# Performance work log

Measured on AMD Instinct MI355X. Metric: run time of the kernel, lower is better.

## Reference

```python
import jax, jax.numpy as jnp
import numpy as np

N_NODES = 50000
N_EDGES = 800000
HIDDEN = 128
NUM_RBF = 32
N_GRAPHS = 500
VOCAB = 100


def setup_inputs() -> dict:
    key = jax.random.key(0)
    ks = jax.random.split(key, 16)
    x = jax.random.randint(ks[0], (N_NODES,), 0, VOCAB)
    edge_index = jax.random.randint(ks[1], (2, N_EDGES), 0, N_NODES)
    edge_attr = jax.random.normal(ks[2], (N_EDGES, NUM_RBF), dtype=jnp.float32)
    batch = jnp.sort(jax.random.randint(ks[3], (N_NODES,), 0, N_GRAPHS))
    zdim = 2 * HIDDEN + NUM_RBF
    s = 1.0 / np.sqrt(zdim)
    params = {"emb": jax.random.normal(ks[4], (VOCAB, HIDDEN), dtype=jnp.float32)}
    for l, k0 in zip((1, 2, 3), (5, 8, 11)):
        params[f"Wf{l}"] = jax.random.uniform(ks[k0], (zdim, HIDDEN), minval=-s, maxval=s, dtype=jnp.float32)
        params[f"bf{l}"] = jnp.zeros((HIDDEN,), dtype=jnp.float32)
        params[f"Ws{l}"] = jax.random.uniform(ks[k0 + 1], (zdim, HIDDEN), minval=-s, maxval=s, dtype=jnp.float32)
        params[f"bs{l}"] = jnp.zeros((HIDDEN,), dtype=jnp.float32)
    sl = 1.0 / np.sqrt(HIDDEN)
    params["Wlin"] = jax.random.uniform(ks[14], (HIDDEN, HIDDEN), minval=-sl, maxval=sl, dtype=jnp.float32)
    params["blin"] = jnp.zeros((HIDDEN,), dtype=jnp.float32)
    return {"x": x, "edge_index": edge_index, "edge_attr": edge_attr, "batch": batch, **params}


def _cgconv(h, src, dst, edge_attr, Wf, bf, Ws, bs):
    # z = [x_i || x_j || e_ij]; i = target (dst), j = source (src)
    z = jnp.concatenate([h[dst], h[src], edge_attr], axis=-1)  # [E, 2H+D]
    msg = jax.nn.sigmoid(z @ Wf + bf) * jax.nn.softplus(z @ Ws + bs)  # [E, H]
    agg = jax.ops.segment_sum(msg, dst, num_segments=N_NODES)
    return h + agg


def reference(x, edge_index, edge_attr, batch, emb,
              Wf1, bf1, Ws1, bs1, Wf2, bf2, Ws2, bs2, Wf3, bf3, Ws3, bs3,
              Wlin, blin):
    src, dst = edge_index[0], edge_index[1]
    h = emb[x]  # [N, H]
    h = jax.nn.relu(_cgconv(h, src, dst, edge_attr, Wf1, bf1, Ws1, bs1))
    h = jax.nn.relu(_cgconv(h, src, dst, edge_attr, Wf2, bf2, Ws2, bs2))
    h = jax.nn.relu(_cgconv(h, src, dst, edge_attr, Wf3, bf3, Ws3, bs3))
    sums = jax.ops.segment_sum(h, batch, num_segments=N_GRAPHS)  # [G, H]
    counts = jax.ops.segment_sum(jnp.ones((N_NODES,), h.dtype), batch, num_segments=N_GRAPHS)
    pooled = sums / jnp.maximum(counts, 1.0)[:, None]
    return pooled @ Wlin + blin
```

## Files before the change

kernel.cpp:

```cpp
#include <hip/hip_runtime.h>
#include <hip/hip_bf16.h>
#include <hip/hip_fp16.h>
#include <cstdint>
#include <cstddef>

#define NNODES 50000
#define NEDGES 800000
#define HID 128
#define NRBF 32
#define NGRAPH 500
#define NB_SCAN 196
#define EPB 32
#define NEBLK (NEDGES / EPB)
#define SROW 130

typedef __attribute__((ext_vector_type(8))) short short8;
typedef __attribute__((ext_vector_type(4))) float f32x4;

__device__ inline short f2bf(float x) {
  __hip_bfloat16 b = __float2bfloat16(x);
  return *reinterpret_cast<short*>(&b);
}

__device__ inline unsigned int pk_bf16(float a, float b) {
  unsigned int r;
  asm("v_cvt_pk_bf16_f32 %0, %1, %2" : "=v"(r) : "v"(a), "v"(b));
  return r;
}
__device__ inline unsigned int pk_f16(float a, float b) {
  unsigned int r;
  asm("v_cvt_pkrtz_f16_f32 %0, %1, %2" : "=v"(r) : "v"(a), "v"(b));
  return r;
}
__device__ inline float aexp2(float x) {
  float r;
  asm("v_exp_f32 %0, %1" : "=v"(r) : "v"(x));
  return r;
}
__device__ inline float alog2(float x) {
  float r;
  asm("v_log_f32 %0, %1" : "=v"(r) : "v"(x));
  return r;
}

#define SC_F (-1.4426950408889634f)
#define SC_S (1.4426950408889634f)

__global__ void prep_all(
    const float* __restrict__ Wf0, const float* __restrict__ Ws0,
    const float* __restrict__ bf0, const float* __restrict__ bs0,
    const float* __restrict__ Wf1, const float* __restrict__ Ws1,
    const float* __restrict__ bf1, const float* __restrict__ bs1,
    const float* __restrict__ Wf2, const float* __restrict__ Ws2,
    const float* __restrict__ bf2, const float* __restrict__ bs2,
    unsigned short* __restrict__ WtB3, unsigned short* __restrict__ WnB3,
    float* __restrict__ biasv3) {
  const int l = blockIdx.y;
  const float* Wf = (l == 0) ? Wf0 : ((l == 1) ? Wf1 : Wf2);
  const float* Ws = (l == 0) ? Ws0 : ((l == 1) ? Ws1 : Ws2);
  const float* bf = (l == 0) ? bf0 : ((l == 1) ? bf1 : bf2);
  const float* bs = (l == 0) ? bs0 : ((l == 1) ? bs1 : bs2);
  unsigned short* WtB = WtB3 + l * 8192;
  unsigned short* WnB = WnB3 + l * 65536;
  float* biasv = biasv3 + l * 256;

  int i0 = blockIdx.x * blockDim.x + threadIdx.x;
  if (i0 < 8192) {
    int i = i0;
    int j = i & 7, lane = (i >> 3) & 63, t = i >> 9;
    int q = lane >> 4, n = lane & 15;
    int k = q * 8 + j, c = (t & 7) * 16 + n;
    const float* W = (t < 8) ? Wf : Ws;
    const float sc = (t < 8) ? SC_F : SC_S;
    WtB[i] = (unsigned short)f2bf(W[(size_t)(256 + k) * HID + c] * sc);
  } else if (i0 < 8192 + 65536) {
    int i = i0 - 8192;
    int j = i & 7;
    int lane = (i >> 3) & 63;
    int tk = (i >> 9) & 3;
    int tc = i >> 11;
    int q = lane >> 4, n = lane & 15;
    int k = tk * 32 + q * 8 + j;
    float v;
    int which;
    if (tc < 16) {
      int cc = tc * 16 + n;
      int c = cc >> 1;
      which = cc & 1;
      const float* W = which ? Ws : Wf;
      v = W[(size_t)k * HID + c];
    } else {
      int g = (tc - 16) >> 1;
      which = (tc - 16) & 1;
      int c = g * 16 + n;
      const float* W = which ? Ws : Wf;
      v = W[(size_t)(128 + k) * HID + c];
    }
    WnB[i] = (unsigned short)f2bf(v * (which ? SC_S : SC_F));
    if (i < 256) {
      int c2 = i >> 1, w2 = i & 1;
      biasv[i] = w2 ? bs[c2] * SC_S : bf[c2] * SC_F;
    }
  }
}

__global__ void deg_hist(const int* __restrict__ dst, int* __restrict__ deg) {
  int e = blockIdx.x * blockDim.x + threadIdx.x;
  if (e < NEDGES) atomicAdd(&deg[dst[e]], 1);
}

__global__ __launch_bounds__(256) void scan_block(const int* __restrict__ deg, int* __restrict__ bsum) {
  __shared__ int s[256];
  int i = blockIdx.x * 256 + threadIdx.x;
  s[threadIdx.x] = (i < NNODES) ? deg[i] : 0;
  __syncthreads();
  for (int off = 128; off > 0; off >>= 1) {
    if (threadIdx.x < off) s[threadIdx.x] += s[threadIdx.x + off];
    __syncthreads();
  }
  if (threadIdx.x == 0) bsum[blockIdx.x] = s[0];
}

__global__ __launch_bounds__(256) void scan_top(const int* __restrict__ bsum,
                                                int* __restrict__ bpre) {
  __shared__ int s[256];
  int t = threadIdx.x;
  int v = (t < NB_SCAN) ? bsum[t] : 0;
  s[t] = v;
  __syncthreads();
  for (int off = 1; off < 256; off <<= 1) {
    int u = (t >= off) ? s[t - off] : 0;
    __syncthreads();
    s[t] += u;
    __syncthreads();
  }
  if (t < NB_SCAN) bpre[t] = s[t] - v;
}

__global__ __launch_bounds__(256) void scan_final(const int* __restrict__ deg,
                                                  const int* __restrict__ bpre,
                                                  int* __restrict__ cursor) {
  __shared__ int s[256];
  int i = blockIdx.x * 256 + threadIdx.x;
  int v = (i < NNODES) ? deg[i] : 0;
  s[threadIdx.x] = v;
  __syncthreads();
  for (int off = 1; off < 256; off <<= 1) {
    int t = (threadIdx.x >= off) ? s[threadIdx.x - off] : 0;
    __syncthreads();
    s[threadIdx.x] += t;
    __syncthreads();
  }
  if (i < NNODES) cursor[i] = bpre[blockIdx.x] + s[threadIdx.x] - v;
}

__global__ void scatter_edges_pack(const int* __restrict__ src, const int* __restrict__ dst,
                                   const float* __restrict__ eattr, int* __restrict__ cursor,
                                   int2* __restrict__ se2, unsigned short* __restrict__ eaB) {
  int e = blockIdx.x * blockDim.x + threadIdx.x;
  if (e >= NEDGES) return;
  int d = dst[e];
  int pos = atomicAdd(&cursor[d], 1);
  se2[pos] = make_int2(src[e], d);
  const float* ep = eattr + (size_t)e * NRBF;
  unsigned short* op = eaB + (size_t)pos * NRBF;
#pragma unroll
  for (int part = 0; part < 4; ++part) {
    const float4 v0 = *(const float4*)&ep[part * 8];
    const float4 v1 = *(const float4*)&ep[part * 8 + 4];
    uint4 o;
    o.x = pk_bf16(v0.x, v0.y);
    o.y = pk_bf16(v0.z, v0.w);
    o.z = pk_bf16(v1.x, v1.y);
    o.w = pk_bf16(v1.z, v1.w);
    *(uint4*)&op[part * 8] = o;
  }
}

__global__ __launch_bounds__(256) void node_mfma(
    const int* __restrict__ x, const float* __restrict__ emb,
    float* __restrict__ h, float* __restrict__ agg,
    const unsigned short* __restrict__ WnB, const float* __restrict__ biasv,
    float* __restrict__ Pdst, unsigned int* __restrict__ Psrc, int mode, int N) {
  const int tid = threadIdx.x;
  const int wv = tid >> 6;
  const int lane = tid & 63;
  const int q = lane >> 4;
  const int n = lane & 15;
  const int nb = blockIdx.x * 32 + (wv >> 1) * 16;
  const int srcwave = wv & 1;
  const int ctile0 = srcwave * 16;

  const bool valid = (nb + n) < N;
  int anode = nb + n;
  if (anode >= N) anode = N - 1;
  float* hp = h + (size_t)anode * HID;

  short8 a[4];
  if (mode == 0) {
    const float* ep = emb + (size_t)x[anode] * HID;
#pragma unroll
    for (int kt = 0; kt < 4; ++kt) {
      const float4 e0 = *(const float4*)&ep[kt * 32 + q * 8];
      const float4 e1 = *(const float4*)&ep[kt * 32 + q * 8 + 4];
      if (valid && !srcwave) {
        *(float4*)&hp[kt * 32 + q * 8] = e0;
        *(float4*)&hp[kt * 32 + q * 8 + 4] = e1;
      }
      union { short8 s8; unsigned int u32[4]; } au;
      au.u32[0] = pk_bf16(e0.x, e0.y);
      au.u32[1] = pk_bf16(e0.z, e0.w);
      au.u32[2] = pk_bf16(e1.x, e1.y);
      au.u32[3] = pk_bf16(e1.z, e1.w);
      a[kt] = au.s8;
    }
  } else {
    float* ap = agg + (size_t)anode * HID;
    float4 ev[8];
#pragma unroll
    for (int kt = 0; kt < 4; ++kt) {
      float4 e0 = *(const float4*)&hp[kt * 32 + q * 8];
      float4 e1 = *(const float4*)&hp[kt * 32 + q * 8 + 4];
      const float4 g0 = *(const float4*)&ap[kt * 32 + q * 8];
      const float4 g1 = *(const float4*)&ap[kt * 32 + q * 8 + 4];
      e0.x = fmaxf(e0.x + g0.x, 0.f); e0.y = fmaxf(e0.y + g0.y, 0.f);
      e0.z = fmaxf(e0.z + g0.z, 0.f); e0.w = fmaxf(e0.w + g0.w, 0.f);
      e1.x = fmaxf(e1.x + g1.x, 0.f); e1.y = fmaxf(e1.y + g1.y, 0.f);
      e1.z = fmaxf(e1.z + g1.z, 0.f); e1.w = fmaxf(e1.w + g1.w, 0.f);
      ev[2 * kt] = e0;
      ev[2 * kt + 1] = e1;
      union { short8 s8; unsigned int u32[4]; } au;
      au.u32[0] = pk_bf16(e0.x, e0.y);
      au.u32[1] = pk_bf16(e0.z, e0.w);
      au.u32[2] = pk_bf16(e1.x, e1.y);
      au.u32[3] = pk_bf16(e1.z, e1.w);
      a[kt] = au.s8;
    }
    __syncthreads();
    if (valid && !srcwave) {
      const float4 z4 = {0.f, 0.f, 0.f, 0.f};
#pragma unroll
      for (int kt = 0; kt < 4; ++kt) {
        *(float4*)&hp[kt * 32 + q * 8] = ev[2 * kt];
        *(float4*)&hp[kt * 32 + q * 8 + 4] = ev[2 * kt + 1];
        *(float4*)&ap[kt * 32 + q * 8] = z4;
        *(float4*)&ap[kt * 32 + q * 8 + 4] = z4;
      }
    }
  }

  const short8* WnB8 = (const short8*)WnB;
  f32x4 acc[16];
#pragma unroll
  for (int tc = 0; tc < 16; ++tc) acc[tc] = (f32x4){0.f, 0.f, 0.f, 0.f};

#pragma unroll
  for (int tc = 0; tc < 16; ++tc) {
#pragma unroll
    for (int kt = 0; kt < 4; ++kt) {
      short8 b = WnB8[((size_t)((ctile0 + tc) * 4 + kt)) * 64 + lane];
      acc[tc] = __builtin_amdgcn_mfma_f32_16x16x32_bf16(a[kt], b, acc[tc], 0, 0, 0);
    }
  }

  if (!srcwave) {
#pragma unroll
    for (int tc = 0; tc < 16; ++tc) {
      const int cout = tc * 16 + n;
      const float bv = biasv[cout];
#pragma unroll
      for (int r = 0; r < 4; ++r) {
        int nd = nb + q * 4 + r;
        if (nd < N) Pdst[(size_t)nd * 256 + cout] = acc[tc][r] + bv;
      }
    }
  } else {
#pragma unroll
    for (int g2 = 0; g2 < 8; ++g2) {
      const int c = g2 * 16 + n;
#pragma unroll
      for (int r = 0; r < 4; ++r) {
        int nd = nb + q * 4 + r;
        if (nd < N) Psrc[(size_t)nd * 128 + c] = pk_f16(acc[2 * g2][r], acc[2 * g2 + 1][r]);
      }
    }
  }
}

__global__ __launch_bounds__(128) void edge_mfma(
    const float* __restrict__ Pdst, const unsigned int* __restrict__ Psrc,
    const unsigned short* __restrict__ eaB, const unsigned short* __restrict__ WtB,
    const int2* __restrict__ se2, float* __restrict__ agg) {
  __shared__ unsigned int fsL[EPB * SROW];
  __shared__ int dstL[EPB];
  __shared__ int grpStart[EPB + 1];
  __shared__ int sndS;

  const int tid = threadIdx.x;
  const int base = blockIdx.x * EPB;
  const int lane = tid & 63;

  if (tid < EPB) {
    int2 sd = se2[base + tid];
    dstL[tid] = sd.y;
    int d = sd.y;
    int dprev = __shfl_up(d, 1);
    int flag = (tid == 0 || dprev != d) ? 1 : 0;
    unsigned long long mask = __ballot(flag);
    int slot = __popcll(mask & ((1ull << (lane + 1)) - 1)) - 1;
    if (flag) grpStart[slot] = tid;
    if (tid == 0) {
      int nd = __popcll(mask);
      sndS = nd;
      grpStart[nd] = EPB;
    }
  }

  const int wv = tid >> 6;
  const int q = lane >> 4;
  const int n = lane & 15;
  const int rowb = wv * 16 + q * 4;

  const short8 afrag = *(const short8*)&eaB[(size_t)(base + wv * 16 + n) * 32 + q * 8];

  const unsigned int* pp[4];
  const float* dp[4];
#pragma unroll
  for (int r = 0; r < 4; ++r) {
    const int2 sd = se2[base + rowb + r];
    pp[r] = Psrc + (size_t)sd.x * 128 + n;
    dp[r] = Pdst + (size_t)sd.y * 256 + 2 * n;
  }

  const short8* WtB8 = (const short8*)WtB;
#pragma unroll
  for (int t = 0; t < 8; ++t) {
    f32x4 cinf, cins;
#pragma unroll
    for (int r = 0; r < 4; ++r) {
      const unsigned int pu = pp[r][t * 16];
      const float2 pd2 = *(const float2*)&dp[r][t * 32];
      const float2 ps = __half22float2(*reinterpret_cast<const __half2*>(&pu));
      cinf[r] = pd2.x + ps.x;
      cins[r] = pd2.y + ps.y;
    }
    short8 bfr = WtB8[t * 64 + lane];
    short8 bsr = WtB8[(8 + t) * 64 + lane];
    f32x4 cf = __builtin_amdgcn_mfma_f32_16x16x32_bf16(afrag, bfr, cinf, 0, 0, 0);
    f32x4 cs = __builtin_amdgcn_mfma_f32_16x16x32_bf16(afrag, bsr, cins, 0, 0, 0);
#pragma unroll
    for (int r = 0; r < 4; ++r) {
      fsL[(rowb + r) * SROW + t * 16 + n] = pk_f16(cf[r], cs[r]);
    }
  }
  __syncthreads();

  const int nd = sndS;
  for (int g = wv; g < nd; g += 2) {
    const int jb = grpStart[g];
    const int je = grpStart[g + 1];
    const int d = __builtin_amdgcn_readfirstlane(dstL[jb]);
    float acc0 = 0.f, acc1 = 0.f;

    uint2 pk_nx = *(const uint2*)&fsL[jb * SROW + 2 * lane];
    for (int j = jb; j < je; ++j) {
      const uint2 pk = pk_nx;
      int jn = (j + 1 < je) ? (j + 1) : j;
      pk_nx = *(const uint2*)&fsL[jn * SROW + 2 * lane];

      const float2 z0 = __half22float2(*reinterpret_cast<const __half2*>(&pk.x));
      const float2 z1 = __half22float2(*reinterpret_cast<const __half2*>(&pk.y));
      const float sig0 = __builtin_amdgcn_rcpf(1.f + aexp2(z0.x));
      const float sig1 = __builtin_amdgcn_rcpf(1.f + aexp2(z1.x));
      const float sp0 = fmaxf(z0.y, 0.f) + alog2(1.f + aexp2(fminf(z0.y, -z0.y)));
      const float sp1 = fmaxf(z1.y, 0.f) + alog2(1.f + aexp2(fminf(z1.y, -z1.y)));
      acc0 = fmaf(sig0, sp0, acc0);
      acc1 = fmaf(sig1, sp1, acc1);
    }
    acc0 *= 0.6931471805599453f;
    acc1 *= 0.6931471805599453f;
    float* ap = agg + (size_t)d * HID + 2 * lane;
    if (g == 0 || g == nd - 1) {
      atomicAdd(ap, acc0);
      atomicAdd(ap + 1, acc1);
    } else {
      *(float2*)ap = make_float2(acc0, acc1);
    }
  }
}

__global__ __launch_bounds__(256) void pool_kernel(
    const float* __restrict__ h, const float* __restrict__ agg,
    const int* __restrict__ batch, float* __restrict__ sums, float* __restrict__ counts) {
  __shared__ int gidL[64];
  __shared__ int grpS[65];
  __shared__ int sndP;

  const int tid = threadIdx.x;
  const int lane = tid & 63;
  const int wv = tid >> 6;
  const int nb = blockIdx.x * 64;
  int nvalid = NNODES - nb;
  if (nvalid > 64) nvalid = 64;

  if (tid < 64) {
    int node = nb + tid;
    int g = batch[node < NNODES ? node : NNODES - 1];
    gidL[tid] = g;
    int gprev = __shfl_up(g, 1);
    int flag = (tid < nvalid && (tid == 0 || gprev != g)) ? 1 : 0;
    unsigned long long mask = __ballot(flag);
    int slot = __popcll(mask & ((lane == 63) ? ~0ull : ((1ull << (lane + 1)) - 1))) - 1;
    if (flag) grpS[slot] = tid;
    if (tid == 0) {
      int nd = __popcll(mask);
      sndP = nd;
      grpS[nd] = nvalid;
    }
  }
  __syncthreads();

  const int nd = sndP;
  for (int g = wv; g < nd; g += 4) {
    const int jb = grpS[g];
    const int je = grpS[g + 1];
    const int gid = __builtin_amdgcn_readfirstlane(gidL[jb]);
    float a0 = 0.f, a1 = 0.f;
    for (int j = jb; j < je; ++j) {
      const float2 hv = *(const float2*)&h[(size_t)(nb + j) * HID + 2 * lane];
      const float2 av = *(const float2*)&agg[(size_t)(nb + j) * HID + 2 * lane];
      a0 += fmaxf(hv.x + av.x, 0.f);
      a1 += fmaxf(hv.y + av.y, 0.f);
    }
    float* sp = sums + (size_t)gid * HID + 2 * lane;
    const bool bnd = (g == 0 || g == nd - 1);
    if (bnd) {
      atomicAdd(sp, a0);
      atomicAdd(sp + 1, a1);
    } else {
      *(float2*)sp = make_float2(a0, a1);
    }
    if (lane == 0) {
      if (bnd) atomicAdd(&counts[gid], (float)(je - jb));
      else counts[gid] = (float)(je - jb);
    }
  }
}

__global__ __launch_bounds__(128) void final_kernel(
    const float* __restrict__ sums, const float* __restrict__ counts,
    const float* __restrict__ Wlin, const float* __restrict__ blin,
    float* __restrict__ out) {
  int g = blockIdx.x;
  int c = threadIdx.x;
  __shared__ float pool[HID];
  float cnt = counts[g];
  cnt = cnt > 1.f ? cnt : 1.f;
  pool[c] = sums[(size_t)g * HID + c] / cnt;
  __syncthreads();
  float acc = blin[c];
#pragma unroll 8
  for (int k = 0; k < HID; ++k) acc = fmaf(pool[k], Wlin[k * HID + c], acc);
  out[(size_t)g * HID + c] = acc;
}

extern "C" void kernel_launch(void* const* d_in, const int* in_sizes, int n_in,
                              void* d_out, int out_size, void* d_ws, size_t ws_size,
                              hipStream_t stream) {
  const int* x = (const int*)d_in[0];
  const int* eidx = (const int*)d_in[1];
  const float* eattr = (const float*)d_in[2];
  const int* batch = (const int*)d_in[3];
  const float* emb = (const float*)d_in[4];
  const float* Wf[3] = {(const float*)d_in[5], (const float*)d_in[9], (const float*)d_in[13]};
  const float* bf[3] = {(const float*)d_in[6], (const float*)d_in[10], (const float*)d_in[14]};
  const float* Ws[3] = {(const float*)d_in[7], (const float*)d_in[11], (const float*)d_in[15]};
  const float* bs[3] = {(const float*)d_in[8], (const float*)d_in[12], (const float*)d_in[16]};
  const float* Wlin = (const float*)d_in[17];
  const float* blin = (const float*)d_in[18];
  const int* srcp = eidx;
  const int* dstp = eidx + NEDGES;

  float* wsf = (float*)d_ws;
  float* h = wsf;
  float* Pdst = h + (size_t)NNODES * HID;
  float* agg = Pdst + (size_t)NNODES * 256;
  float* sums = agg + (size_t)NNODES * HID;
  float* counts = sums + (size_t)NGRAPH * HID;
  float* biasv3 = counts + NGRAPH;
  unsigned int* Psrc = (unsigned int*)(biasv3 + 768);
  unsigned short* WtB3 = (unsigned short*)(Psrc + (size_t)NNODES * 128);
  unsigned short* WnB3 = WtB3 + 3 * 8192;
  unsigned short* eaB = WnB3 + 3 * 65536;
  int2* se2 = (int2*)(eaB + (size_t)NEDGES * 32);
  int* deg = (int*)(se2 + NEDGES);
  int* cursor = deg + NNODES;
  int* bsum = cursor + NNODES;
  int* bpre = bsum + NB_SCAN;

  dim3 pgrid(288, 3);
  prep_all<<<pgrid, 256, 0, stream>>>(Wf[0], Ws[0], bf[0], bs[0],
                                      Wf[1], Ws[1], bf[1], bs[1],
                                      Wf[2], Ws[2], bf[2], bs[2],
                                      WtB3, WnB3, biasv3);

  hipMemsetAsync(deg, 0, NNODES * sizeof(int), stream);
  deg_hist<<<(NEDGES + 255) / 256, 256, 0, stream>>>(dstp, deg);
  scan_block<<<NB_SCAN, 256, 0, stream>>>(deg, bsum);
  scan_top<<<1, 256, 0, stream>>>(bsum, bpre);
  scan_final<<<NB_SCAN, 256, 0, stream>>>(deg, bpre, cursor);
  scatter_edges_pack<<<(NEDGES + 255) / 256, 256, 0, stream>>>(srcp, dstp, eattr, cursor,
                                                               se2, eaB);

  hipMemsetAsync(agg, 0, (size_t)NNODES * HID * sizeof(float), stream);

  const int nblk_node = (NNODES + 31) / 32;
  for (int l = 0; l < 3; ++l) {
    node_mfma<<<nblk_node, 256, 0, stream>>>(x, emb, h, agg, WnB3 + l * 65536,
                                             biasv3 + l * 256, Pdst, Psrc,
                                             l > 0 ? 1 : 0, NNODES);
    edge_mfma<<<NEBLK, 128, 0, stream>>>(Pdst, Psrc, eaB, WtB3 + l * 8192, se2, agg);
  }

  hipMemsetAsync(sums, 0, (size_t)(NGRAPH * HID + NGRAPH) * sizeof(float), stream);
  pool_kernel<<<(NNODES + 63) / 64, 256, 0, stream>>>(h, agg, batch, sums, counts);
  final_kernel<<<NGRAPH, 128, 0, stream>>>(sums, counts, Wlin, blin, (float*)d_out);
}
```

Measured before the change: 831.0 us.

## Store Pdst as packed fp16 and double edges per block with 256 threads

Node projections for the destination side are now stored as packed fp16 pairs (gate, softplus channel) instead of fp32, halving the per-edge gather traffic from Pdst. The edge kernel adds the gathered src and dst projections with a packed fp16 add and applies them after the MFMA rather than as the accumulator input. It also doubles edges per block to 64 with 4 waves, which means more destination-group sharing and fewer atomics per block. This trades precision (fp16 accumulation of pre-activations) for bandwidth, and the weight prep layout and ballot mask are adjusted to fit the new interleaving and 64-wide wave.

```diff
diff --git a/kernel.cpp b/kernel.cpp
--- a/kernel.cpp
+++ b/kernel.cpp
@@ -10,7 +10,7 @@
 #define NRBF 32
 #define NGRAPH 500
 #define NB_SCAN 196
-#define EPB 32
+#define EPB 64
 #define NEBLK (NEDGES / EPB)
 #define SROW 130
 
@@ -30,6 +30,11 @@
 __device__ inline unsigned int pk_f16(float a, float b) {
   unsigned int r;
   asm("v_cvt_pkrtz_f16_f32 %0, %1, %2" : "=v"(r) : "v"(a), "v"(b));
+  return r;
+}
+__device__ inline unsigned int pk_add_f16(unsigned int a, unsigned int b) {
+  unsigned int r;
+  asm("v_pk_add_f16 %0, %1, %2" : "=v"(r) : "v"(a), "v"(b));
   return r;
 }
 __device__ inline float aexp2(float x) {
@@ -84,9 +89,9 @@
     float v;
     int which;
     if (tc < 16) {
-      int cc = tc * 16 + n;
-      int c = cc >> 1;
-      which = cc & 1;
+      int g = tc >> 1;
+      which = tc & 1;
+      int c = g * 16 + n;
       const float* W = which ? Ws : Wf;
       v = W[(size_t)k * HID + c];
     } else {
@@ -181,7 +186,7 @@
     const int* __restrict__ x, const float* __restrict__ emb,
     float* __restrict__ h, float* __restrict__ agg,
     const unsigned short* __restrict__ WnB, const float* __restrict__ biasv,
-    float* __restrict__ Pdst, unsigned int* __restrict__ Psrc, int mode, int N) {
+    unsigned int* __restrict__ Pdst, unsigned int* __restrict__ Psrc, int mode, int N) {
   const int tid = threadIdx.x;
   const int wv = tid >> 6;
   const int lane = tid & 63;
@@ -265,13 +270,15 @@
 
   if (!srcwave) {
 #pragma unroll
-    for (int tc = 0; tc < 16; ++tc) {
-      const int cout = tc * 16 + n;
-      const float bv = biasv[cout];
+    for (int g2 = 0; g2 < 8; ++g2) {
+      const int c = g2 * 16 + n;
+      const float bvf = biasv[2 * c];
+      const float bvs = biasv[2 * c + 1];
 #pragma unroll
       for (int r = 0; r < 4; ++r) {
         int nd = nb + q * 4 + r;
-        if (nd < N) Pdst[(size_t)nd * 256 + cout] = acc[tc][r] + bv;
+        if (nd < N)
+          Pdst[(size_t)nd * 128 + c] = pk_f16(acc[2 * g2][r] + bvf, acc[2 * g2 + 1][r] + bvs);
       }
     }
   } else {
@@ -287,8 +294,8 @@
   }
 }
 
-__global__ __launch_bounds__(128) void edge_mfma(
-    const float* __restrict__ Pdst, const unsigned int* __restrict__ Psrc,
+__global__ __launch_bounds__(256) void edge_mfma(
+    const unsigned int* __restrict__ Pdst, const unsigned int* __restrict__ Psrc,
     const unsigned short* __restrict__ eaB, const unsigned short* __restrict__ WtB,
     const int2* __restrict__ se2, float* __restrict__ agg) {
   __shared__ unsigned int fsL[EPB * SROW];
@@ -307,7 +314,8 @@
     int dprev = __shfl_up(d, 1);
     int flag = (tid == 0 || dprev != d) ? 1 : 0;
     unsigned long long mask = __ballot(flag);
-    int slot = __popcll(mask & ((1ull << (lane + 1)) - 1)) - 1;
+    unsigned long long below = (lane == 63) ? ~0ull : ((1ull << (lane + 1)) - 1);
+    int slot = __popcll(mask & below) - 1;
     if (flag) grpStart[slot] = tid;
     if (tid == 0) {
       int nd = __popcll(mask);
@@ -324,39 +332,34 @@
   const short8 afrag = *(const short8*)&eaB[(size_t)(base + wv * 16 + n) * 32 + q * 8];
 
   const unsigned int* pp[4];
-  const float* dp[4];
+  const unsigned int* dp[4];
 #pragma unroll
   for (int r = 0; r < 4; ++r) {
     const int2 sd = se2[base + rowb + r];
     pp[r] = Psrc + (size_t)sd.x * 128 + n;
-    dp[r] = Pdst + (size_t)sd.y * 256 + 2 * n;
+    dp[r] = Pdst + (size_t)sd.y * 128 + n;
   }
 
   const short8* WtB8 = (const short8*)WtB;
+  const f32x4 zero4 = {0.f, 0.f, 0.f, 0.f};
 #pragma unroll
   for (int t = 0; t < 8; ++t) {
-    f32x4 cinf, cins;
-#pragma unroll
-    for (int r = 0; r < 4; ++r) {
-      const unsigned int pu = pp[r][t * 16];
-      const float2 pd2 = *(const float2*)&dp[r][t * 32];
-      const float2 ps = __half22float2(*reinterpret_cast<const __half2*>(&pu));
-      cinf[r] = pd2.x + ps.x;
-      cins[r] = pd2.y + ps.y;
-    }
+    unsigned int zpk[4];
+#pragma unroll
+    for (int r = 0; r < 4; ++r) zpk[r] = pk_add_f16(pp[r][t * 16], dp[r][t * 16]);
     short8 bfr = WtB8[t * 64 + lane];
     short8 bsr = WtB8[(8 + t) * 64 + lane];
-    f32x4 cf = __builtin_amdgcn_mfma_f32_16x16x32_bf16(afrag, bfr, cinf, 0, 0, 0);
-    f32x4 cs = __builtin_amdgcn_mfma_f32_16x16x32_bf16(afrag, bsr, cins, 0, 0, 0);
+    f32x4 cf = __builtin_amdgcn_mfma_f32_16x16x32_bf16(afrag, bfr, zero4, 0, 0, 0);
+    f32x4 cs = __builtin_amdgcn_mfma_f32_16x16x32_bf16(afrag, bsr, zero4, 0, 0, 0);
 #pragma unroll
     for (int r = 0; r < 4; ++r) {
-      fsL[(rowb + r) * SROW + t * 16 + n] = pk_f16(cf[r], cs[r]);
+      fsL[(rowb + r) * SROW + t * 16 + n] = pk_add_f16(pk_f16(cf[r], cs[r]), zpk[r]);
     }
   }
   __syncthreads();
 
   const int nd = sndS;
-  for (int g = wv; g < nd; g += 2) {
+  for (int g = wv; g < nd; g += 4) {
     const int jb = grpStart[g];
     const int je = grpStart[g + 1];
     const int d = __builtin_amdgcn_readfirstlane(dstL[jb]);
@@ -483,8 +486,8 @@
 
   float* wsf = (float*)d_ws;
   float* h = wsf;
-  float* Pdst = h + (size_t)NNODES * HID;
-  float* agg = Pdst + (size_t)NNODES * 256;
+  float* PdstF = h + (size_t)NNODES * HID;
+  float* agg = PdstF + (size_t)NNODES * 256;
   float* sums = agg + (size_t)NNODES * HID;
   float* counts = sums + (size_t)NGRAPH * HID;
   float* biasv3 = counts + NGRAPH;
@@ -497,6 +500,7 @@
   int* cursor = deg + NNODES;
   int* bsum = cursor + NNODES;
   int* bpre = bsum + NB_SCAN;
+  unsigned int* Pdst = (unsigned int*)PdstF;
 
   dim3 pgrid(288, 3);
   prep_all<<<pgrid, 256, 0, stream>>>(Wf[0], Ws[0], bf[0], bs[0],
@@ -519,7 +523,7 @@
     node_mfma<<<nblk_node, 256, 0, stream>>>(x, emb, h, agg, WnB3 + l * 65536,
                                              biasv3 + l * 256, Pdst, Psrc,
                                              l > 0 ? 1 : 0, NNODES);
-    edge_mfma<<<NEBLK, 128, 0, stream>>>(Pdst, Psrc, eaB, WtB3 + l * 8192, se2, agg);
+    edge_mfma<<<NEBLK, 256, 0, stream>>>(Pdst, Psrc, eaB, WtB3 + l * 8192, se2, agg);
   }
 
   hipMemsetAsync(sums, 0, (size_t)(NGRAPH * HID + NGRAPH) * sizeof(float), stream);
```

After: 736.1 us. -11.4%, faster.
